# Performance work log

Measured on AMD Instinct MI355X. Metric: run time of the kernel, lower is better.

The kernel has to match this reference:

```python
import jax, jax.numpy as jnp
import numpy as np

N, E = 100000, 1600000
D_IN, H1, D1 = 512, 8, 16   # layer0: 8 heads x 16 = hidden 128
H2, D2 = 1, 64              # layer1: 1 head x 64
SLOPE = 0.2


def setup_inputs() -> dict:
    key = jax.random.key(0)
    ks = jax.random.split(key, 9)
    feats = jax.random.normal(ks[0], (N, D_IN), dtype=jnp.float32)
    src = jax.random.randint(ks[1], (E,), 0, N, dtype=jnp.int32)
    dst = jax.random.randint(ks[2], (E,), 0, N, dtype=jnp.int32)
    s = 0.05
    W1 = jax.random.normal(ks[3], (H1 * D1, D_IN), dtype=jnp.float32) * s
    al1 = jax.random.normal(ks[4], (1, H1, D1), dtype=jnp.float32) * s
    ar1 = jax.random.normal(ks[5], (1, H1, D1), dtype=jnp.float32) * s
    W2 = jax.random.normal(ks[6], (H2 * D2, H1 * D1), dtype=jnp.float32) * s
    al2 = jax.random.normal(ks[7], (1, H2, D2), dtype=jnp.float32) * s
    ar2 = jax.random.normal(ks[8], (1, H2, D2), dtype=jnp.float32) * s
    return {"feats": feats, "src": src, "dst": dst,
            "W1": W1, "al1": al1, "ar1": ar1,
            "W2": W2, "al2": al2, "ar2": ar2}


def _segment_softmax(e, seg, n):
    # e: [E, H], softmax over edges sharing the same destination node
    m = jax.ops.segment_max(e, seg, num_segments=n)
    m = jax.lax.stop_gradient(m)
    ex = jnp.exp(e - m[seg])
    s = jax.ops.segment_sum(ex, seg, num_segments=n)
    return ex / s[seg]


def _gat_conv(feat, W, al, ar, src, dst):
    n = feat.shape[0]
    h, d = al.shape[1], al.shape[2]
    ft = (feat @ W.T).reshape(n, h, d)          # [N, H, D]
    el = jnp.sum(ft * al, axis=-1)               # [N, H]
    er = jnp.sum(ft * ar, axis=-1)               # [N, H]
    e = el[src] + er[dst]                        # [E, H]
    e = jnp.where(e >= 0, e, SLOPE * e)          # leaky_relu
    a = _segment_softmax(e, dst, n)              # [E, H]
    msg = ft[src] * a[:, :, None]                # [E, H, D]
    rst = jax.ops.segment_sum(msg, dst, num_segments=n)  # [N, H, D]
    return rst, a


def reference(feats, src, dst, W1, al1, ar1, W2, al2, ar2):
    # layer 0 (activation=relu inside GATConv), then flatten heads
    h1, _ = _gat_conv(feats, W1, al1, ar1, src, dst)
    h1 = jax.nn.relu(h1).reshape(feats.shape[0], -1)    # [N, H1*D1]
    # output layer (1 head, no activation), then mean over heads
    h2, _ = _gat_conv(h1, W2, al2, ar2, src, dst)
    h = h2.mean(axis=1)                                  # [N, D2]
    # forward returns (h_list, h) with h_list = [feats, h1]
    return (feats, h1, h)
```

## Files before the change

kernel.cpp:

```cpp
#include <hip/hip_runtime.h>
#include <math.h>

#define N_NODES 100000
#define N_EDGES 1600000
#define D_IN 512
#define C1 128
#define H1 8
#define D2 64
#define SLOPE 0.2f
#define NB_SCAN 98

typedef unsigned short u16;
typedef unsigned int u32;
typedef u16 u16x4 __attribute__((ext_vector_type(4)));
typedef u16 u16x8 __attribute__((ext_vector_type(8)));
typedef short bf16x8 __attribute__((ext_vector_type(8)));
typedef float f32x4 __attribute__((ext_vector_type(4)));

__device__ __forceinline__ u16 f2bf(float f) {
    unsigned u = __builtin_bit_cast(unsigned, f);
    u += 0x7fffu + ((u >> 16) & 1u);
    return (u16)(u >> 16);
}
__device__ __forceinline__ float bf2f(u16 v) {
    unsigned u = ((unsigned)v) << 16;
    return __builtin_bit_cast(float, u);
}
__device__ __forceinline__ float bflo(u32 u) { return __builtin_bit_cast(float, u << 16); }
__device__ __forceinline__ float bfhi(u32 u) { return __builtin_bit_cast(float, u & 0xffff0000u); }
__device__ __forceinline__ float lrelu(float e) { return e >= 0.f ? e : SLOPE * e; }

__global__ void k_prep_w1(const float* __restrict__ W1, u16* __restrict__ W1b) {
    int i = blockIdx.x * blockDim.x + threadIdx.x;
    float4 v = ((const float4*)W1)[i];
    u16x4 b; b.x = f2bf(v.x); b.y = f2bf(v.y); b.z = f2bf(v.z); b.w = f2bf(v.w);
    ((u16x4*)W1b)[i] = b;
}

__global__ void k_hist(const int* __restrict__ dst, int* __restrict__ cnt) {
    int e = blockIdx.x * blockDim.x + threadIdx.x;
    if (e < N_EDGES) atomicAdd(&cnt[dst[e]], 1);
}

__global__ void k_scan_partials(const int* __restrict__ cnt, int* __restrict__ partials) {
    __shared__ int s[256];
    int t = threadIdx.x;
    int base = blockIdx.x * 1024 + t * 4;
    int sum = 0;
#pragma unroll
    for (int j = 0; j < 4; j++) { int i = base + j; if (i < N_NODES) sum += cnt[i]; }
    s[t] = sum;
    __syncthreads();
    for (int off = 128; off > 0; off >>= 1) {
        if (t < off) s[t] += s[t + off];
        __syncthreads();
    }
    if (t == 0) partials[blockIdx.x] = s[0];
}

__global__ void k_scan_offsets(const int* __restrict__ partials, int* __restrict__ offsets,
                               int* __restrict__ row_start) {
    __shared__ int s[128];
    int t = threadIdx.x;
    int v = (t < NB_SCAN) ? partials[t] : 0;
    s[t] = v;
    __syncthreads();
    for (int off = 1; off < 128; off <<= 1) {
        int x = (t >= off) ? s[t - off] : 0;
        __syncthreads();
        s[t] += x;
        __syncthreads();
    }
    if (t < NB_SCAN) offsets[t] = s[t] - v;
    if (t == NB_SCAN - 1) row_start[N_NODES] = s[t];
}

__global__ void k_scan_final(const int* __restrict__ cnt, const int* __restrict__ offsets,
                             int* __restrict__ row_start, int* __restrict__ cursor) {
    __shared__ int s[256];
    int t = threadIdx.x;
    int base = blockIdx.x * 1024 + t * 4;
    int v[4];
    int sum = 0;
#pragma unroll
    for (int j = 0; j < 4; j++) {
        int i = base + j;
        v[j] = (i < N_NODES) ? cnt[i] : 0;
        sum += v[j];
    }
    s[t] = sum;
    __syncthreads();
    for (int off = 1; off < 256; off <<= 1) {
        int x = (t >= off) ? s[t - off] : 0;
        __syncthreads();
        s[t] += x;
        __syncthreads();
    }
    int b = offsets[blockIdx.x] + s[t] - sum;
    int e = 0;
#pragma unroll
    for (int j = 0; j < 4; j++) {
        int i = base + j;
        if (i < N_NODES) { row_start[i] = b + e; cursor[i] = b + e; }
        e += v[j];
    }
}

__global__ void k_scatter(const int* __restrict__ src, const int* __restrict__ dst,
                          int* __restrict__ cursor, int* __restrict__ csr_src) {
    int e = blockIdx.x * blockDim.x + threadIdx.x;
    if (e < N_EDGES) {
        int pos = atomicAdd(&cursor[dst[e]], 1);
        csr_src[pos] = src[e];
    }
}

__global__ __launch_bounds__(256) void k_gemm1(const float* __restrict__ feats,
                                               const u16* __restrict__ W1b,
                                               u16* __restrict__ ft1b,
                                               float* __restrict__ out0) {
    __shared__ u16 As[64 * 40];
    __shared__ u16 Bs[128 * 40];
    int t = threadIdx.x;
    int m0 = blockIdx.x * 64;
    int wave = t >> 6, lane = t & 63, quad = lane >> 4, mr = lane & 15;

    f32x4 acc[8];
#pragma unroll
    for (int i = 0; i < 8; i++)
#pragma unroll
        for (int j = 0; j < 4; j++) acc[i][j] = 0.f;

    for (int kt = 0; kt < D_IN; kt += 32) {
        __syncthreads();
#pragma unroll
        for (int l = 0; l < 2; ++l) {
            int idx = t + l * 256;
            int row = idx >> 3, k4 = idx & 7;
            int n = m0 + row;
            float4 v = make_float4(0.f, 0.f, 0.f, 0.f);
            if (n < N_NODES) {
                v = *(const float4*)(feats + (size_t)n * D_IN + kt + k4 * 4);
                *(float4*)(out0 + (size_t)n * D_IN + kt + k4 * 4) = v;
            }
            u16x4 b; b.x = f2bf(v.x); b.y = f2bf(v.y); b.z = f2bf(v.z); b.w = f2bf(v.w);
            *(u16x4*)(As + row * 40 + k4 * 4) = b;
        }
#pragma unroll
        for (int l = 0; l < 2; ++l) {
            int idx = t + l * 256;
            int o = idx >> 2, k8 = idx & 3;
            *(u16x8*)(Bs + o * 40 + k8 * 8) = *(const u16x8*)(W1b + (size_t)o * D_IN + kt + k8 * 8);
        }
        __syncthreads();
        bf16x8 a = *(const bf16x8*)(As + (wave * 16 + mr) * 40 + quad * 8);
#pragma unroll
        for (int nt = 0; nt < 8; ++nt) {
            bf16x8 b = *(const bf16x8*)(Bs + (nt * 16 + mr) * 40 + quad * 8);
            acc[nt] = __builtin_amdgcn_mfma_f32_16x16x32_bf16(a, b, acc[nt], 0, 0, 0);
        }
    }
#pragma unroll
    for (int nt = 0; nt < 8; ++nt)
#pragma unroll
        for (int r = 0; r < 4; ++r) {
            int n = m0 + wave * 16 + quad * 4 + r;
            if (n < N_NODES) ft1b[(size_t)n * C1 + nt * 16 + mr] = f2bf(acc[nt][r]);
        }
}

__global__ void k_eler1(const u16* __restrict__ ft1b, const float* __restrict__ al1,
                        const float* __restrict__ ar1, float* __restrict__ el1,
                        float* __restrict__ er1) {
    int g = blockIdx.x * blockDim.x + threadIdx.x;
    if (g >= N_NODES * H1) return;
    int n = g >> 3, h = g & 7;
    const u16* f = ft1b + (size_t)n * C1 + h * 16;
    float sl = 0.f, sr = 0.f;
#pragma unroll
    for (int d = 0; d < 16; ++d) {
        float v = bf2f(f[d]);
        sl = fmaf(v, al1[h * 16 + d], sl);
        sr = fmaf(v, ar1[h * 16 + d], sr);
    }
    el1[g] = sl;
    er1[g] = sr;
}

__global__ __launch_bounds__(256) void k_agg1(const u16* __restrict__ ft1b,
                                              const float* __restrict__ el1,
                                              const float* __restrict__ er1,
                                              const int* __restrict__ row_start,
                                              const int* __restrict__ csr_src,
                                              float* __restrict__ h1out,
                                              u32* __restrict__ h1b) {
    int lane = threadIdx.x & 63;
    int n = blockIdx.x * 4 + (threadIdx.x >> 6);
    if (n >= N_NODES) return;
    int h = lane >> 3;
    float era = er1[n * 8 + h];
    int beg = row_start[n], end = row_start[n + 1];
    float a0 = 0.f, a1 = 0.f, sw = 0.f;
    const u32* ftp = (const u32*)ft1b;
    int i = beg;
    for (; i + 4 <= end; i += 4) {
        int s0 = csr_src[i + 0], s1 = csr_src[i + 1];
        int s2 = csr_src[i + 2], s3 = csr_src[i + 3];
        float e0 = el1[s0 * 8 + h], e1 = el1[s1 * 8 + h];
        float e2 = el1[s2 * 8 + h], e3 = el1[s3 * 8 + h];
        u32 f0 = ftp[s0 * 64 + lane], f1 = ftp[s1 * 64 + lane];
        u32 f2 = ftp[s2 * 64 + lane], f3 = ftp[s3 * 64 + lane];
        float w0 = __expf(lrelu(e0 + era));
        float w1 = __expf(lrelu(e1 + era));
        float w2 = __expf(lrelu(e2 + era));
        float w3 = __expf(lrelu(e3 + era));
        a0 = fmaf(w0, bflo(f0), a0); a1 = fmaf(w0, bfhi(f0), a1);
        a0 = fmaf(w1, bflo(f1), a0); a1 = fmaf(w1, bfhi(f1), a1);
        a0 = fmaf(w2, bflo(f2), a0); a1 = fmaf(w2, bfhi(f2), a1);
        a0 = fmaf(w3, bflo(f3), a0); a1 = fmaf(w3, bfhi(f3), a1);
        sw += w0 + w1 + w2 + w3;
    }
    for (; i < end; ++i) {
        int s = csr_src[i];
        float e = el1[s * 8 + h];
        u32 f = ftp[s * 64 + lane];
        float w = __expf(lrelu(e + era));
        a0 = fmaf(w, bflo(f), a0); a1 = fmaf(w, bfhi(f), a1);
        sw += w;
    }
    float r0 = (sw > 0.f) ? fmaxf(a0 / sw, 0.f) : 0.f;
    float r1 = (sw > 0.f) ? fmaxf(a1 / sw, 0.f) : 0.f;
    float2 rr; rr.x = r0; rr.y = r1;
    *(float2*)(h1out + (size_t)n * C1 + 2 * lane) = rr;
    h1b[n * 64 + lane] = (u32)f2bf(r0) | ((u32)f2bf(r1) << 16);
}

__global__ __launch_bounds__(256) void k_gemm2(const u16* __restrict__ h1b,
                                               const float* __restrict__ W2,
                                               u16* __restrict__ ft2b) {
    __shared__ u16 As[128 * 136];
    __shared__ u16 Bs[64 * 136];
    int t = threadIdx.x;
    int n0 = blockIdx.x * 128;
#pragma unroll
    for (int l = 0; l < 8; ++l) {
        int idx = t + l * 256;
        int row = idx >> 4, c8 = idx & 15;
        int n = n0 + row;
        u16x8 v;
#pragma unroll
        for (int j = 0; j < 8; j++) v[j] = 0;
        if (n < N_NODES) v = *(const u16x8*)(h1b + (size_t)n * C1 + c8 * 8);
        *(u16x8*)(As + row * 136 + c8 * 8) = v;
    }
#pragma unroll
    for (int l = 0; l < 8; ++l) {
        int idx = t + l * 256;
        int o = idx >> 5, k4 = idx & 31;
        float4 w = *(const float4*)(W2 + (size_t)o * C1 + k4 * 4);
        u16x4 b; b.x = f2bf(w.x); b.y = f2bf(w.y); b.z = f2bf(w.z); b.w = f2bf(w.w);
        *(u16x4*)(Bs + o * 136 + k4 * 4) = b;
    }
    __syncthreads();
    int wave = t >> 6, lane = t & 63, quad = lane >> 4, mr = lane & 15;
    f32x4 acc[2][4];
#pragma unroll
    for (int i = 0; i < 2; i++)
#pragma unroll
        for (int j = 0; j < 4; j++)
#pragma unroll
            for (int r = 0; r < 4; r++) acc[i][j][r] = 0.f;
#pragma unroll
    for (int kc = 0; kc < 4; ++kc) {
        bf16x8 a0 = *(const bf16x8*)(As + (wave * 32 + mr) * 136 + kc * 32 + quad * 8);
        bf16x8 a1 = *(const bf16x8*)(As + (wave * 32 + 16 + mr) * 136 + kc * 32 + quad * 8);
#pragma unroll
        for (int nt = 0; nt < 4; ++nt) {
            bf16x8 b = *(const bf16x8*)(Bs + (nt * 16 + mr) * 136 + kc * 32 + quad * 8);
            acc[0][nt] = __builtin_amdgcn_mfma_f32_16x16x32_bf16(a0, b, acc[0][nt], 0, 0, 0);
            acc[1][nt] = __builtin_amdgcn_mfma_f32_16x16x32_bf16(a1, b, acc[1][nt], 0, 0, 0);
        }
    }
#pragma unroll
    for (int mf = 0; mf < 2; ++mf)
#pragma unroll
        for (int nt = 0; nt < 4; ++nt)
#pragma unroll
            for (int r = 0; r < 4; ++r) {
                int n = n0 + wave * 32 + mf * 16 + quad * 4 + r;
                if (n < N_NODES) ft2b[(size_t)n * D2 + nt * 16 + mr] = f2bf(acc[mf][nt][r]);
            }
}

__global__ void k_eler2(const u16* __restrict__ ft2b, const float* __restrict__ al2,
                        const float* __restrict__ ar2, float* __restrict__ el2,
                        float* __restrict__ er2) {
    int lane = threadIdx.x & 63;
    int n = blockIdx.x * 4 + (threadIdx.x >> 6);
    if (n >= N_NODES) return;
    float v = bf2f(ft2b[(size_t)n * D2 + lane]);
    float p = v * al2[lane];
    float q = v * ar2[lane];
#pragma unroll
    for (int off = 32; off > 0; off >>= 1) {
        p += __shfl_down(p, off, 64);
        q += __shfl_down(q, off, 64);
    }
    if (lane == 0) { el2[n] = p; er2[n] = q; }
}

__global__ __launch_bounds__(256) void k_agg2(const u16* __restrict__ ft2b,
                                              const float* __restrict__ el2,
                                              const float* __restrict__ er2,
                                              const int* __restrict__ row_start,
                                              const int* __restrict__ csr_src,
                                              float* __restrict__ out2) {
    int lane = threadIdx.x & 63;
    int n = blockIdx.x * 4 + (threadIdx.x >> 6);
    if (n >= N_NODES) return;
    int half = lane >> 5;
    int c = (lane & 31) * 2;
    float ern = er2[n];
    int beg = row_start[n], end = row_start[n + 1];
    float a0 = 0.f, a1 = 0.f, sw = 0.f;
    const u32* ftp = (const u32*)ft2b;
    int i = beg + half;
    for (; i + 2 < end; i += 4) {
        int s0 = csr_src[i], s1 = csr_src[i + 2];
        float e0 = el2[s0], e1 = el2[s1];
        u32 f0 = ftp[s0 * 32 + (lane & 31)], f1 = ftp[s1 * 32 + (lane & 31)];
        float w0 = __expf(lrelu(e0 + ern));
        float w1 = __expf(lrelu(e1 + ern));
        a0 = fmaf(w0, bflo(f0), a0); a1 = fmaf(w0, bfhi(f0), a1);
        a0 = fmaf(w1, bflo(f1), a0); a1 = fmaf(w1, bfhi(f1), a1);
        sw += w0 + w1;
    }
    for (; i < end; i += 2) {
        int s = csr_src[i];
        float e = el2[s];
        u32 f = ftp[s * 32 + (lane & 31)];
        float w = __expf(lrelu(e + ern));
        a0 = fmaf(w, bflo(f), a0); a1 = fmaf(w, bfhi(f), a1);
        sw += w;
    }
    a0 += __shfl_xor(a0, 32, 64);
    a1 += __shfl_xor(a1, 32, 64);
    sw += __shfl_xor(sw, 32, 64);
    if (half == 0) {
        float2 rr;
        rr.x = (sw > 0.f) ? a0 / sw : 0.f;
        rr.y = (sw > 0.f) ? a1 / sw : 0.f;
        *(float2*)(out2 + (size_t)n * D2 + c) = rr;
    }
}

extern "C" void kernel_launch(void* const* d_in, const int* in_sizes, int n_in,
                              void* d_out, int out_size, void* d_ws, size_t ws_size,
                              hipStream_t stream) {
    const float* feats = (const float*)d_in[0];
    const int* src = (const int*)d_in[1];
    const int* dst = (const int*)d_in[2];
    const float* W1 = (const float*)d_in[3];
    const float* al1 = (const float*)d_in[4];
    const float* ar1 = (const float*)d_in[5];
    const float* W2 = (const float*)d_in[6];
    const float* al2 = (const float*)d_in[7];
    const float* ar2 = (const float*)d_in[8];

    float* out0 = (float*)d_out;
    float* out1 = out0 + (size_t)N_NODES * D_IN;
    float* out2 = out1 + (size_t)N_NODES * C1;

    char* ws = (char*)d_ws;
    size_t off = 0;
    auto alloc = [&](size_t bytes) -> void* {
        void* p = ws + off;
        off = (off + bytes + 255) & ~(size_t)255;
        return p;
    };
    u16* ft1b = (u16*)alloc((size_t)N_NODES * C1 * 2);
    u16* h1b = (u16*)alloc((size_t)N_NODES * C1 * 2);
    u16* ft2b = (u16*)alloc((size_t)N_NODES * D2 * 2);
    u16* W1b = (u16*)alloc((size_t)C1 * D_IN * 2);
    float* el1 = (float*)alloc((size_t)N_NODES * H1 * 4);
    float* er1 = (float*)alloc((size_t)N_NODES * H1 * 4);
    float* el2 = (float*)alloc((size_t)N_NODES * 4);
    float* er2 = (float*)alloc((size_t)N_NODES * 4);
    int* cnt = (int*)alloc((size_t)N_NODES * 4);
    int* row_start = (int*)alloc((size_t)(N_NODES + 1) * 4);
    int* cursor = (int*)alloc((size_t)N_NODES * 4);
    int* csr_src = (int*)alloc((size_t)N_EDGES * 4);
    int* partials = (int*)alloc((size_t)NB_SCAN * 4);
    int* offsets = (int*)alloc((size_t)NB_SCAN * 4);

    hipMemsetAsync(cnt, 0, (size_t)N_NODES * 4, stream);
    k_hist<<<(N_EDGES + 255) / 256, 256, 0, stream>>>(dst, cnt);
    k_scan_partials<<<NB_SCAN, 256, 0, stream>>>(cnt, partials);
    k_scan_offsets<<<1, 128, 0, stream>>>(partials, offsets, row_start);
    k_scan_final<<<NB_SCAN, 256, 0, stream>>>(cnt, offsets, row_start, cursor);
    k_scatter<<<(N_EDGES + 255) / 256, 256, 0, stream>>>(src, dst, cursor, csr_src);

    k_prep_w1<<<64, 256, 0, stream>>>(W1, W1b);

    k_gemm1<<<(N_NODES + 63) / 64, 256, 0, stream>>>(feats, W1b, ft1b, out0);
    k_eler1<<<(N_NODES * H1 + 255) / 256, 256, 0, stream>>>(ft1b, al1, ar1, el1, er1);
    k_agg1<<<(N_NODES + 3) / 4, 256, 0, stream>>>(ft1b, el1, er1, row_start, csr_src, out1, (u32*)h1b);

    k_gemm2<<<(N_NODES + 127) / 128, 256, 0, stream>>>(h1b, W2, ft2b);
    k_eler2<<<(N_NODES + 3) / 4, 256, 0, stream>>>(ft2b, al2, ar2, el2, er2);
    k_agg2<<<(N_NODES + 3) / 4, 256, 0, stream>>>(ft2b, el2, er2, row_start, csr_src, out2);
}
```

Baseline: 824.4 us.

## Fuse attention logit dot-products into GEMM epilogues and batch edge gathers via wave shuffles

Computes el/er for both layers directly from the MFMA accumulators in the GEMM epilogues, so the separate k_eler1 and k_eler2 kernels are removed. Layer-1 el/er are interleaved into one [N,16] buffer. The aggregation loops now load 64 CSR indices per wave in one coalesced read and broadcast them with shuffles, then issue 8 (or 4) independent gathers at a time to expose memory-level parallelism. The cost is extra shuffle reductions in the GEMM epilogues and masked wasted work for low-degree tails. The logits now come from fp32 accumulators rather than bf16-rounded features.

```diff
diff --git a/kernel.cpp b/kernel.cpp
--- a/kernel.cpp
+++ b/kernel.cpp
@@ -117,8 +117,11 @@
 
 __global__ __launch_bounds__(256) void k_gemm1(const float* __restrict__ feats,
                                                const u16* __restrict__ W1b,
+                                               const float* __restrict__ al1,
+                                               const float* __restrict__ ar1,
                                                u16* __restrict__ ft1b,
-                                               float* __restrict__ out0) {
+                                               float* __restrict__ out0,
+                                               float* __restrict__ eler1) {
     __shared__ u16 As[64 * 40];
     __shared__ u16 Bs[128 * 40];
     int t = threadIdx.x;
@@ -167,29 +170,32 @@
             int n = m0 + wave * 16 + quad * 4 + r;
             if (n < N_NODES) ft1b[(size_t)n * C1 + nt * 16 + mr] = f2bf(acc[nt][r]);
         }
-}
-
-__global__ void k_eler1(const u16* __restrict__ ft1b, const float* __restrict__ al1,
-                        const float* __restrict__ ar1, float* __restrict__ el1,
-                        float* __restrict__ er1) {
-    int g = blockIdx.x * blockDim.x + threadIdx.x;
-    if (g >= N_NODES * H1) return;
-    int n = g >> 3, h = g & 7;
-    const u16* f = ft1b + (size_t)n * C1 + h * 16;
-    float sl = 0.f, sr = 0.f;
-#pragma unroll
-    for (int d = 0; d < 16; ++d) {
-        float v = bf2f(f[d]);
-        sl = fmaf(v, al1[h * 16 + d], sl);
-        sr = fmaf(v, ar1[h * 16 + d], sr);
-    }
-    el1[g] = sl;
-    er1[g] = sr;
+    float al1v[8], ar1v[8];
+#pragma unroll
+    for (int nt = 0; nt < 8; ++nt) { al1v[nt] = al1[nt * 16 + mr]; ar1v[nt] = ar1[nt * 16 + mr]; }
+#pragma unroll
+    for (int r = 0; r < 4; ++r) {
+        int n = m0 + wave * 16 + quad * 4 + r;
+        float sel = 0.f;
+#pragma unroll
+        for (int nt = 0; nt < 8; ++nt) {
+            float v = acc[nt][r];
+            float pl = v * al1v[nt];
+            float pr = v * ar1v[nt];
+#pragma unroll
+            for (int off = 1; off < 16; off <<= 1) {
+                pl += __shfl_xor(pl, off, 64);
+                pr += __shfl_xor(pr, off, 64);
+            }
+            sel = (mr == nt) ? pl : sel;
+            sel = (mr == nt + 8) ? pr : sel;
+        }
+        if (n < N_NODES) eler1[(size_t)n * 16 + mr] = sel;
+    }
 }
 
 __global__ __launch_bounds__(256) void k_agg1(const u16* __restrict__ ft1b,
-                                              const float* __restrict__ el1,
-                                              const float* __restrict__ er1,
+                                              const float* __restrict__ eler1,
                                               const int* __restrict__ row_start,
                                               const int* __restrict__ csr_src,
                                               float* __restrict__ h1out,
@@ -198,35 +204,36 @@
     int n = blockIdx.x * 4 + (threadIdx.x >> 6);
     if (n >= N_NODES) return;
     int h = lane >> 3;
-    float era = er1[n * 8 + h];
+    float era = eler1[(size_t)n * 16 + 8 + h];
     int beg = row_start[n], end = row_start[n + 1];
     float a0 = 0.f, a1 = 0.f, sw = 0.f;
     const u32* ftp = (const u32*)ft1b;
-    int i = beg;
-    for (; i + 4 <= end; i += 4) {
-        int s0 = csr_src[i + 0], s1 = csr_src[i + 1];
-        int s2 = csr_src[i + 2], s3 = csr_src[i + 3];
-        float e0 = el1[s0 * 8 + h], e1 = el1[s1 * 8 + h];
-        float e2 = el1[s2 * 8 + h], e3 = el1[s3 * 8 + h];
-        u32 f0 = ftp[s0 * 64 + lane], f1 = ftp[s1 * 64 + lane];
-        u32 f2 = ftp[s2 * 64 + lane], f3 = ftp[s3 * 64 + lane];
-        float w0 = __expf(lrelu(e0 + era));
-        float w1 = __expf(lrelu(e1 + era));
-        float w2 = __expf(lrelu(e2 + era));
-        float w3 = __expf(lrelu(e3 + era));
-        a0 = fmaf(w0, bflo(f0), a0); a1 = fmaf(w0, bfhi(f0), a1);
-        a0 = fmaf(w1, bflo(f1), a0); a1 = fmaf(w1, bfhi(f1), a1);
-        a0 = fmaf(w2, bflo(f2), a0); a1 = fmaf(w2, bfhi(f2), a1);
-        a0 = fmaf(w3, bflo(f3), a0); a1 = fmaf(w3, bfhi(f3), a1);
-        sw += w0 + w1 + w2 + w3;
-    }
-    for (; i < end; ++i) {
-        int s = csr_src[i];
-        float e = el1[s * 8 + h];
-        u32 f = ftp[s * 64 + lane];
-        float w = __expf(lrelu(e + era));
-        a0 = fmaf(w, bflo(f), a0); a1 = fmaf(w, bfhi(f), a1);
-        sw += w;
+    for (int base = beg; base < end; base += 64) {
+        int rem = end - base;
+        int sv = csr_src[base + ((lane < rem) ? lane : 0)];
+        int cnt = rem < 64 ? rem : 64;
+        for (int j = 0; j < cnt; j += 8) {
+            int s[8];
+#pragma unroll
+            for (int kk = 0; kk < 8; ++kk) {
+                int idx = j + kk;
+                int sl = (idx < cnt) ? idx : j;
+                s[kk] = __shfl(sv, sl, 64);
+            }
+            float e[8];
+#pragma unroll
+            for (int kk = 0; kk < 8; ++kk) e[kk] = eler1[(size_t)s[kk] * 16 + h];
+            u32 f[8];
+#pragma unroll
+            for (int kk = 0; kk < 8; ++kk) f[kk] = ftp[(size_t)s[kk] * 64 + lane];
+#pragma unroll
+            for (int kk = 0; kk < 8; ++kk) {
+                float w = ((j + kk) < cnt) ? __expf(lrelu(e[kk] + era)) : 0.f;
+                a0 = fmaf(w, bflo(f[kk]), a0);
+                a1 = fmaf(w, bfhi(f[kk]), a1);
+                sw += w;
+            }
+        }
     }
     float r0 = (sw > 0.f) ? fmaxf(a0 / sw, 0.f) : 0.f;
     float r1 = (sw > 0.f) ? fmaxf(a1 / sw, 0.f) : 0.f;
@@ -237,7 +244,11 @@
 
 __global__ __launch_bounds__(256) void k_gemm2(const u16* __restrict__ h1b,
                                                const float* __restrict__ W2,
-                                               u16* __restrict__ ft2b) {
+                                               const float* __restrict__ al2,
+                                               const float* __restrict__ ar2,
+                                               u16* __restrict__ ft2b,
+                                               float* __restrict__ el2,
+                                               float* __restrict__ er2) {
     __shared__ u16 As[128 * 136];
     __shared__ u16 Bs[64 * 136];
     int t = threadIdx.x;
@@ -290,23 +301,28 @@
                 int n = n0 + wave * 32 + mf * 16 + quad * 4 + r;
                 if (n < N_NODES) ft2b[(size_t)n * D2 + nt * 16 + mr] = f2bf(acc[mf][nt][r]);
             }
-}
-
-__global__ void k_eler2(const u16* __restrict__ ft2b, const float* __restrict__ al2,
-                        const float* __restrict__ ar2, float* __restrict__ el2,
-                        float* __restrict__ er2) {
-    int lane = threadIdx.x & 63;
-    int n = blockIdx.x * 4 + (threadIdx.x >> 6);
-    if (n >= N_NODES) return;
-    float v = bf2f(ft2b[(size_t)n * D2 + lane]);
-    float p = v * al2[lane];
-    float q = v * ar2[lane];
-#pragma unroll
-    for (int off = 32; off > 0; off >>= 1) {
-        p += __shfl_down(p, off, 64);
-        q += __shfl_down(q, off, 64);
-    }
-    if (lane == 0) { el2[n] = p; er2[n] = q; }
+    float al2v[4], ar2v[4];
+#pragma unroll
+    for (int nt = 0; nt < 4; ++nt) { al2v[nt] = al2[nt * 16 + mr]; ar2v[nt] = ar2[nt * 16 + mr]; }
+#pragma unroll
+    for (int mf = 0; mf < 2; ++mf)
+#pragma unroll
+        for (int r = 0; r < 4; ++r) {
+            int n = n0 + wave * 32 + mf * 16 + quad * 4 + r;
+            float pl = 0.f, pr = 0.f;
+#pragma unroll
+            for (int nt = 0; nt < 4; ++nt) {
+                float v = acc[mf][nt][r];
+                pl = fmaf(v, al2v[nt], pl);
+                pr = fmaf(v, ar2v[nt], pr);
+            }
+#pragma unroll
+            for (int off = 1; off < 16; off <<= 1) {
+                pl += __shfl_xor(pl, off, 64);
+                pr += __shfl_xor(pr, off, 64);
+            }
+            if (mr == 0 && n < N_NODES) { el2[n] = pl; er2[n] = pr; }
+        }
 }
 
 __global__ __launch_bounds__(256) void k_agg2(const u16* __restrict__ ft2b,
@@ -324,24 +340,32 @@
     int beg = row_start[n], end = row_start[n + 1];
     float a0 = 0.f, a1 = 0.f, sw = 0.f;
     const u32* ftp = (const u32*)ft2b;
-    int i = beg + half;
-    for (; i + 2 < end; i += 4) {
-        int s0 = csr_src[i], s1 = csr_src[i + 2];
-        float e0 = el2[s0], e1 = el2[s1];
-        u32 f0 = ftp[s0 * 32 + (lane & 31)], f1 = ftp[s1 * 32 + (lane & 31)];
-        float w0 = __expf(lrelu(e0 + ern));
-        float w1 = __expf(lrelu(e1 + ern));
-        a0 = fmaf(w0, bflo(f0), a0); a1 = fmaf(w0, bfhi(f0), a1);
-        a0 = fmaf(w1, bflo(f1), a0); a1 = fmaf(w1, bfhi(f1), a1);
-        sw += w0 + w1;
-    }
-    for (; i < end; i += 2) {
-        int s = csr_src[i];
-        float e = el2[s];
-        u32 f = ftp[s * 32 + (lane & 31)];
-        float w = __expf(lrelu(e + ern));
-        a0 = fmaf(w, bflo(f), a0); a1 = fmaf(w, bfhi(f), a1);
-        sw += w;
+    for (int base = beg; base < end; base += 64) {
+        int rem = end - base;
+        int sv = csr_src[base + ((lane < rem) ? lane : 0)];
+        int cnt = rem < 64 ? rem : 64;
+        for (int j = 0; j < cnt; j += 8) {
+            int s[4];
+#pragma unroll
+            for (int kk = 0; kk < 4; ++kk) {
+                int idx = j + 2 * kk + half;
+                int sl = (idx < cnt) ? idx : j;
+                s[kk] = __shfl(sv, sl, 64);
+            }
+            float e[4];
+#pragma unroll
+            for (int kk = 0; kk < 4; ++kk) e[kk] = el2[s[kk]];
+            u32 f[4];
+#pragma unroll
+            for (int kk = 0; kk < 4; ++kk) f[kk] = ftp[(size_t)s[kk] * 32 + (lane & 31)];
+#pragma unroll
+            for (int kk = 0; kk < 4; ++kk) {
+                float w = ((j + 2 * kk + half) < cnt) ? __expf(lrelu(e[kk] + ern)) : 0.f;
+                a0 = fmaf(w, bflo(f[kk]), a0);
+                a1 = fmaf(w, bfhi(f[kk]), a1);
+                sw += w;
+            }
+        }
     }
     a0 += __shfl_xor(a0, 32, 64);
     a1 += __shfl_xor(a1, 32, 64);
@@ -382,8 +406,7 @@
     u16* h1b = (u16*)alloc((size_t)N_NODES * C1 * 2);
     u16* ft2b = (u16*)alloc((size_t)N_NODES * D2 * 2);
     u16* W1b = (u16*)alloc((size_t)C1 * D_IN * 2);
-    float* el1 = (float*)alloc((size_t)N_NODES * H1 * 4);
-    float* er1 = (float*)alloc((size_t)N_NODES * H1 * 4);
+    float* eler1 = (float*)alloc((size_t)N_NODES * 16 * 4);
     float* el2 = (float*)alloc((size_t)N_NODES * 4);
     float* er2 = (float*)alloc((size_t)N_NODES * 4);
     int* cnt = (int*)alloc((size_t)N_NODES * 4);
@@ -402,11 +425,9 @@
 
     k_prep_w1<<<64, 256, 0, stream>>>(W1, W1b);
 
-    k_gemm1<<<(N_NODES + 63) / 64, 256, 0, stream>>>(feats, W1b, ft1b, out0);
-    k_eler1<<<(N_NODES * H1 + 255) / 256, 256, 0, stream>>>(ft1b, al1, ar1, el1, er1);
-    k_agg1<<<(N_NODES + 3) / 4, 256, 0, stream>>>(ft1b, el1, er1, row_start, csr_src, out1, (u32*)h1b);
-
-    k_gemm2<<<(N_NODES + 127) / 128, 256, 0, stream>>>(h1b, W2, ft2b);
-    k_eler2<<<(N_NODES + 3) / 4, 256, 0, stream>>>(ft2b, al2, ar2, el2, er2);
+    k_gemm1<<<(N_NODES + 63) / 64, 256, 0, stream>>>(feats, W1b, al1, ar1, ft1b, out0, eler1);
+    k_agg1<<<(N_NODES + 3) / 4, 256, 0, stream>>>(ft1b, eler1, row_start, csr_src, out1, (u32*)h1b);
+
+    k_gemm2<<<(N_NODES + 127) / 128, 256, 0, stream>>>(h1b, W2, al2, ar2, ft2b, el2, er2);
     k_agg2<<<(N_NODES + 3) / 4, 256, 0, stream>>>(ft2b, el2, er2, row_start, csr_src, out2);
 }
```

New measurement: 794.3 us. -3.6%, faster.
